# Kernel tuning notes

Hardware: AMD Instinct MI355X
Metric: run time of the kernel (lower is better)

The kernel has to match this reference:

```python
import jax, jax.numpy as jnp
import numpy as np

N_NODES = 50000
N_EDGES = 600000
IN_F = 256
OUT_F = 128


def setup_inputs() -> dict:
    key = jax.random.key(0)
    k1, k2, k3, k4, k5, k6 = jax.random.split(key, 6)
    x = jax.random.normal(k1, (N_NODES, IN_F), dtype=jnp.float32)
    edge_rows = jax.random.randint(k2, (N_EDGES,), 0, N_NODES, dtype=jnp.int32)
    edge_cols = jax.random.randint(k3, (N_EDGES,), 0, N_NODES, dtype=jnp.int32)
    edge_vals = jax.random.uniform(k4, (N_EDGES,), dtype=jnp.float32)
    # xavier_uniform init bound for weight [in, out]
    bound = float(np.sqrt(6.0 / (IN_F + OUT_F)))
    weight = jax.random.uniform(k5, (IN_F, OUT_F), dtype=jnp.float32, minval=-bound, maxval=bound)
    bias = jax.random.normal(k6, (OUT_F,), dtype=jnp.float32) * 0.02
    return {"x": x, "edge_rows": edge_rows, "edge_cols": edge_cols,
            "edge_vals": edge_vals, "weight": weight, "bias": bias}


def reference(x, edge_rows, edge_cols, edge_vals, weight, bias):
    # support = x @ W            [N, out]
    support = x @ weight
    # sparse adj @ support: out[r] += val * support[c] for each edge (r, c, val)
    msgs = edge_vals[:, None] * support[edge_cols]           # [E, out]
    agg = jax.ops.segment_sum(msgs, edge_rows, num_segments=N_NODES)  # [N, out]
    return agg + bias
```

## Files before the change

### kernel.cpp

```cpp
#include <hip/hip_runtime.h>
#include <hip/hip_bf16.h>

#define N_NODES 50000
#define N_EDGES 600000
#define IN_F 256
#define OUT_F 128
#define GEMM_BLOCKS 196
#define NBUCK 782
#define NBUCKA 784
#define BROWS 64
#define NBLK_E 256
#define EPB 2344
#define ITERS 5
#define CAP 1024

typedef __bf16 bf16x8 __attribute__((ext_vector_type(8)));
typedef __bf16 bf16x4 __attribute__((ext_vector_type(4)));
typedef __bf16 bf16x2 __attribute__((ext_vector_type(2)));
typedef float  f32x4  __attribute__((ext_vector_type(4)));

#define GLOAD(P, ks)                                    \
    P##_0 = *(const float4*)(xp0 + (ks) * 32);          \
    P##_1 = *(const float4*)(xp0 + (ks) * 32 + 4);      \
    P##_2 = *(const float4*)(xp1 + (ks) * 32);          \
    P##_3 = *(const float4*)(xp1 + (ks) * 32 + 4);

#define KSTEP(P, ks) {                                                             \
    bf16x8 af0 = { (__bf16)P##_0.x, (__bf16)P##_0.y, (__bf16)P##_0.z, (__bf16)P##_0.w, \
                   (__bf16)P##_1.x, (__bf16)P##_1.y, (__bf16)P##_1.z, (__bf16)P##_1.w };\
    bf16x8 af1 = { (__bf16)P##_2.x, (__bf16)P##_2.y, (__bf16)P##_2.z, (__bf16)P##_2.w, \
                   (__bf16)P##_3.x, (__bf16)P##_3.y, (__bf16)P##_3.z, (__bf16)P##_3.w };\
    _Pragma("unroll")                                                              \
    for (int nt = 0; nt < 8; nt++) {                                               \
        int nrow = nt * 16 + m;                                                    \
        const bf16x8 bf = *(const bf16x8*)(smem + (nrow << 9) +                    \
                            (((ks) * 64 + quad * 16) ^ ((nrow & 7) << 4)));        \
        acc0[nt] = __builtin_amdgcn_mfma_f32_16x16x32_bf16(af0, bf, acc0[nt], 0, 0, 0); \
        acc1[nt] = __builtin_amdgcn_mfma_f32_16x16x32_bf16(af1, bf, acc1[nt], 0, 0, 0); \
    } }

__global__ __launch_bounds__(512, 3) void gcn_gemm_scatter(const float* __restrict__ x,
                                                           const float* __restrict__ w,
                                                           __bf16* __restrict__ support,
                                                           const int* __restrict__ erows,
                                                           const int* __restrict__ ecols,
                                                           const float* __restrict__ evals,
                                                           int* __restrict__ cursor,
                                                           int2* __restrict__ bucketed) {
    __shared__ char smem[65536];
    const int t = threadIdx.x;

    if (blockIdx.x >= GEMM_BLOCKS) {
        int b = blockIdx.x - GEMM_BLOCKS;
        int* lh = (int*)smem;
        for (int j = t; j < NBUCKA; j += 512) lh[j] = 0;
        __syncthreads();
        int e0 = b * EPB;
        int e1 = e0 + EPB; if (e1 > N_EDGES) e1 = N_EDGES;
        int myr[ITERS];
#pragma unroll
        for (int j = 0; j < ITERS; j++) {
            int e = e0 + j * 512 + t;
            myr[j] = -1;
            if (e < e1) {
                int r = erows[e];
                myr[j] = r;
                atomicAdd(&lh[r >> 6], 1);
            }
        }
        __syncthreads();
        for (int j0 = t; j0 < NBUCKA; j0 += 512) {
            int c = lh[j0];
            lh[j0] = c ? atomicAdd(&cursor[j0], c) : 0;
        }
        __syncthreads();
#pragma unroll
        for (int j = 0; j < ITERS; j++) {
            int r = myr[j];
            if (r >= 0) {
                int e = e0 + j * 512 + t;
                int g = r >> 6;
                int rank = atomicAdd(&lh[g], 1);
                if (rank < CAP)
                    bucketed[((size_t)g << 10) + rank] =
                        make_int2(((r & 63) << 16) | ecols[e],
                                  __float_as_int(evals[e]));
            }
        }
        return;
    }

    const int wave = t >> 6;
    const int lane = t & 63;
    const int m    = lane & 15;
    const int quad = lane >> 4;

    {
        int n  = t & 127;
        int kb = (t >> 7) * 4;
        int xorv = (n & 7) << 4;
        char* ldsrow = smem + (n << 9);
#pragma unroll 4
        for (int j = 0; j < 16; j++) {
            int k = kb + 16 * j;
            float a0 = w[(k + 0) * OUT_F + n];
            float a1 = w[(k + 1) * OUT_F + n];
            float a2 = w[(k + 2) * OUT_F + n];
            float a3 = w[(k + 3) * OUT_F + n];
            bf16x4 pk = { (__bf16)a0, (__bf16)a1, (__bf16)a2, (__bf16)a3 };
            *(bf16x4*)(ldsrow + ((2 * k) ^ xorv)) = pk;
        }
    }

    const int row0 = blockIdx.x * 256 + wave * 32;
    int r0 = row0 + m;
    int r1 = row0 + 16 + m;
    const float* xp0 = x + (size_t)(r0 < N_NODES ? r0 : 0) * IN_F + quad * 8;
    const float* xp1 = x + (size_t)(r1 < N_NODES ? r1 : 0) * IN_F + quad * 8;

    f32x4 acc0[8], acc1[8];
#pragma unroll
    for (int nt = 0; nt < 8; nt++) {
        acc0[nt] = (f32x4){0.f, 0.f, 0.f, 0.f};
        acc1[nt] = (f32x4){0.f, 0.f, 0.f, 0.f};
    }

    __syncthreads();

    float4 A_0, A_1, A_2, A_3, B_0, B_1, B_2, B_3, C_0, C_1, C_2, C_3;
    GLOAD(A, 0) GLOAD(B, 1)
    GLOAD(C, 2) KSTEP(A, 0)
    GLOAD(A, 3) KSTEP(B, 1)
    GLOAD(B, 4) KSTEP(C, 2)
    GLOAD(C, 5) KSTEP(A, 3)
    GLOAD(A, 6) KSTEP(B, 4)
    GLOAD(B, 7) KSTEP(C, 5)
    KSTEP(A, 6)
    KSTEP(B, 7)

    __syncthreads();
#pragma unroll
    for (int nt = 0; nt < 8; nt++) {
        int cb = (nt * 16 + m) * 2;
#pragma unroll
        for (int r = 0; r < 4; r++) {
            int lr0 = wave * 32 + quad * 4 + r;
            int lr1 = lr0 + 16;
            *(__bf16*)(smem + (lr0 << 8) + (cb ^ ((lr0 & 7) << 4))) = (__bf16)acc0[nt][r];
            *(__bf16*)(smem + (lr1 << 8) + (cb ^ ((lr1 & 7) << 4))) = (__bf16)acc1[nt][r];
        }
    }
    __syncthreads();
    {
        int row  = t >> 1;
        int half = t & 1;
        int g = blockIdx.x * 256 + row;
        if (g < N_NODES) {
            char* dst = (char*)(support + (size_t)g * OUT_F) + half * 128;
#pragma unroll
            for (int j = 0; j < 8; j++) {
                int boff = (half * 128 + j * 16) ^ ((row & 7) << 4);
                *(bf16x8*)(dst + j * 16) = *(const bf16x8*)(smem + (row << 8) + boff);
            }
        }
    }
}

__global__ __launch_bounds__(512, 8) void gcn_agg_sorted(const __bf16* __restrict__ support,
                                                         const int2* __restrict__ bucketed,
                                                         const int* __restrict__ cursor,
                                                         const float* __restrict__ bias,
                                                         float* __restrict__ out) {
    __shared__ int2 se_raw[CAP];
    __shared__ int2 se[CAP];
    __shared__ int  lh[BROWS];
    __shared__ int  rs[BROWS];
    __shared__ int  run[BROWS];
    __shared__ int  sc[128];
    const int g  = blockIdx.x;
    const int t  = threadIdx.x;
    const int wv = t >> 6, ln = t & 63;

    const int beg = g << 10;
    int ne = cursor[g]; if (ne > CAP) ne = CAP; if (ne < 0) ne = 0;

    if (t < BROWS) lh[t] = 0;
    __syncthreads();
    for (int i = t; i < ne; i += 512) {
        int2 cv = bucketed[beg + i];
        se_raw[i] = cv;
        atomicAdd(&lh[cv.x >> 16], 1);
    }
    __syncthreads();

    if (t < 128) {
        int v = (t < BROWS) ? lh[t] : 0;
        sc[t] = v;
    }
    __syncthreads();
#pragma unroll
    for (int off = 1; off < BROWS; off <<= 1) {
        int x = 0;
        if (t < 128 && t >= off) x = sc[t - off];
        __syncthreads();
        if (t < 128) sc[t] += x;
        __syncthreads();
    }
    if (t < BROWS) {
        int v = lh[t];
        rs[t] = sc[t] - v;
        run[t] = sc[t] - v;
    }
    __syncthreads();

    for (int i = t; i < ne; i += 512) {
        int2 cv = se_raw[i];
        int p = atomicAdd(&run[cv.x >> 16], 1);
        se[p] = make_int2(cv.x & 0xFFFF, cv.y);
    }
    __syncthreads();

    const int grow0 = g * BROWS;
    const __bf16* spL = support + ln * 2;
    const float2 bias2 = *(const float2*)&bias[ln * 2];
    for (int rr = 0; rr < 8; rr++) {
        int row  = wv * 8 + rr;
        int grow = grow0 + row;
        if (grow >= N_NODES) break;
        float2 acc = bias2;
        float2 accB = make_float2(0.f, 0.f);
        int b0 = rs[row];
        int b1 = b0 + lh[row];
        int j = b0;
        for (; j + 7 < b1; j += 8) {
            int2 e0 = se[j];
            int2 e1 = se[j + 1];
            int2 e2 = se[j + 2];
            int2 e3 = se[j + 3];
            int2 e4 = se[j + 4];
            int2 e5 = se[j + 5];
            int2 e6 = se[j + 6];
            int2 e7 = se[j + 7];
            bf16x2 s0 = *(const bf16x2*)(spL + (size_t)e0.x * OUT_F);
            bf16x2 s1 = *(const bf16x2*)(spL + (size_t)e1.x * OUT_F);
            bf16x2 s2 = *(const bf16x2*)(spL + (size_t)e2.x * OUT_F);
            bf16x2 s3 = *(const bf16x2*)(spL + (size_t)e3.x * OUT_F);
            bf16x2 s4 = *(const bf16x2*)(spL + (size_t)e4.x * OUT_F);
            bf16x2 s5 = *(const bf16x2*)(spL + (size_t)e5.x * OUT_F);
            bf16x2 s6 = *(const bf16x2*)(spL + (size_t)e6.x * OUT_F);
            bf16x2 s7 = *(const bf16x2*)(spL + (size_t)e7.x * OUT_F);
            float v0 = __int_as_float(e0.y);
            float v1 = __int_as_float(e1.y);
            float v2 = __int_as_float(e2.y);
            float v3 = __int_as_float(e3.y);
            float v4 = __int_as_float(e4.y);
            float v5 = __int_as_float(e5.y);
            float v6 = __int_as_float(e6.y);
            float v7 = __int_as_float(e7.y);
            acc.x  += v0 * (float)s0.x + v1 * (float)s1.x;
            acc.y  += v0 * (float)s0.y + v1 * (float)s1.y;
            accB.x += v2 * (float)s2.x + v3 * (float)s3.x;
            accB.y += v2 * (float)s2.y + v3 * (float)s3.y;
            acc.x  += v4 * (float)s4.x + v5 * (float)s5.x;
            acc.y  += v4 * (float)s4.y + v5 * (float)s5.y;
            accB.x += v6 * (float)s6.x + v7 * (float)s7.x;
            accB.y += v6 * (float)s6.y + v7 * (float)s7.y;
        }
        for (; j + 3 < b1; j += 4) {
            int2 e0 = se[j];
            int2 e1 = se[j + 1];
            int2 e2 = se[j + 2];
            int2 e3 = se[j + 3];
            bf16x2 s0 = *(const bf16x2*)(spL + (size_t)e0.x * OUT_F);
            bf16x2 s1 = *(const bf16x2*)(spL + (size_t)e1.x * OUT_F);
            bf16x2 s2 = *(const bf16x2*)(spL + (size_t)e2.x * OUT_F);
            bf16x2 s3 = *(const bf16x2*)(spL + (size_t)e3.x * OUT_F);
            float v0 = __int_as_float(e0.y);
            float v1 = __int_as_float(e1.y);
            float v2 = __int_as_float(e2.y);
            float v3 = __int_as_float(e3.y);
            acc.x  += v0 * (float)s0.x + v1 * (float)s1.x;
            acc.y  += v0 * (float)s0.y + v1 * (float)s1.y;
            accB.x += v2 * (float)s2.x + v3 * (float)s3.x;
            accB.y += v2 * (float)s2.y + v3 * (float)s3.y;
        }
        for (; j < b1; j++) {
            int2 e0 = se[j];
            bf16x2 s0 = *(const bf16x2*)(spL + (size_t)e0.x * OUT_F);
            float v0 = __int_as_float(e0.y);
            acc.x += v0 * (float)s0.x;
            acc.y += v0 * (float)s0.y;
        }
        acc.x += accB.x;
        acc.y += accB.y;
        *(float2*)&out[(size_t)grow * OUT_F + ln * 2] = acc;
    }
}

static inline size_t align_up(size_t v, size_t a) { return (v + a - 1) & ~(a - 1); }

extern "C" void kernel_launch(void* const* d_in, const int* in_sizes, int n_in,
                              void* d_out, int out_size, void* d_ws, size_t ws_size,
                              hipStream_t stream) {
    const float* x     = (const float*)d_in[0];
    const int*   erows = (const int*)d_in[1];
    const int*   ecols = (const int*)d_in[2];
    const float* evals = (const float*)d_in[3];
    const float* w     = (const float*)d_in[4];
    const float* bias  = (const float*)d_in[5];
    float* out = (float*)d_out;

    size_t off = 0;
    __bf16* support   = (__bf16*)((char*)d_ws + off);
    off = align_up(off + (size_t)N_NODES * OUT_F * 2, 64);
    int*    cursor    = (int*)((char*)d_ws + off);
    off = align_up(off + (size_t)NBUCKA * 4, 64);
    int2*   bucketed  = (int2*)((char*)d_ws + off);

    hipMemsetAsync(cursor, 0, (size_t)NBUCKA * sizeof(int), stream);

    gcn_gemm_scatter<<<GEMM_BLOCKS + NBLK_E, 512, 0, stream>>>(
        x, w, support, erows, ecols, evals, cursor, bucketed);

    gcn_agg_sorted<<<NBUCK, 512, 0, stream>>>(support, bucketed, cursor, bias, out);
}
```

Before: 142.5 us.

## Halve per-block rows in GEMM and split aggregation buckets across two blocks

The GEMM phase now gives each wave 16 rows instead of 32, so twice as many blocks are launched but each reuses the staged weight tile half as often. The aggregation kernel launches two blocks per 64-row bucket. Each block keeps only the edges for its 32-row half, which adds an overflow cap. The goal is more parallelism on a GPU with many CUs, at the cost of re-staging the weights more often and scanning each bucket's edge list twice.

```diff
diff --git a/kernel.cpp b/kernel.cpp
--- a/kernel.cpp
+++ b/kernel.cpp
@@ -5,14 +5,16 @@
 #define N_EDGES 600000
 #define IN_F 256
 #define OUT_F 128
-#define GEMM_BLOCKS 196
+#define GEMM_BLOCKS 392
 #define NBUCK 782
 #define NBUCKA 784
 #define BROWS 64
+#define AGG_BLOCKS 1564
 #define NBLK_E 256
 #define EPB 2344
 #define ITERS 5
 #define CAP 1024
+#define HCAP 512
 
 typedef __bf16 bf16x8 __attribute__((ext_vector_type(8)));
 typedef __bf16 bf16x4 __attribute__((ext_vector_type(4)));
@@ -21,22 +23,17 @@
 
 #define GLOAD(P, ks)                                    \
     P##_0 = *(const float4*)(xp0 + (ks) * 32);          \
-    P##_1 = *(const float4*)(xp0 + (ks) * 32 + 4);      \
-    P##_2 = *(const float4*)(xp1 + (ks) * 32);          \
-    P##_3 = *(const float4*)(xp1 + (ks) * 32 + 4);
+    P##_1 = *(const float4*)(xp0 + (ks) * 32 + 4);
 
 #define KSTEP(P, ks) {                                                             \
     bf16x8 af0 = { (__bf16)P##_0.x, (__bf16)P##_0.y, (__bf16)P##_0.z, (__bf16)P##_0.w, \
                    (__bf16)P##_1.x, (__bf16)P##_1.y, (__bf16)P##_1.z, (__bf16)P##_1.w };\
-    bf16x8 af1 = { (__bf16)P##_2.x, (__bf16)P##_2.y, (__bf16)P##_2.z, (__bf16)P##_2.w, \
-                   (__bf16)P##_3.x, (__bf16)P##_3.y, (__bf16)P##_3.z, (__bf16)P##_3.w };\
     _Pragma("unroll")                                                              \
     for (int nt = 0; nt < 8; nt++) {                                               \
         int nrow = nt * 16 + m;                                                    \
         const bf16x8 bf = *(const bf16x8*)(smem + (nrow << 9) +                    \
                             (((ks) * 64 + quad * 16) ^ ((nrow & 7) << 4)));        \
         acc0[nt] = __builtin_amdgcn_mfma_f32_16x16x32_bf16(af0, bf, acc0[nt], 0, 0, 0); \
-        acc1[nt] = __builtin_amdgcn_mfma_f32_16x16x32_bf16(af1, bf, acc1[nt], 0, 0, 0); \
     } }
 
 __global__ __launch_bounds__(512, 3) void gcn_gemm_scatter(const float* __restrict__ x,
@@ -112,22 +109,18 @@
         }
     }
 
-    const int row0 = blockIdx.x * 256 + wave * 32;
+    const int row0 = blockIdx.x * 128 + wave * 16;
     int r0 = row0 + m;
-    int r1 = row0 + 16 + m;
     const float* xp0 = x + (size_t)(r0 < N_NODES ? r0 : 0) * IN_F + quad * 8;
-    const float* xp1 = x + (size_t)(r1 < N_NODES ? r1 : 0) * IN_F + quad * 8;
-
-    f32x4 acc0[8], acc1[8];
-#pragma unroll
-    for (int nt = 0; nt < 8; nt++) {
+
+    f32x4 acc0[8];
+#pragma unroll
+    for (int nt = 0; nt < 8; nt++)
         acc0[nt] = (f32x4){0.f, 0.f, 0.f, 0.f};
-        acc1[nt] = (f32x4){0.f, 0.f, 0.f, 0.f};
-    }
-
-    __syncthreads();
-
-    float4 A_0, A_1, A_2, A_3, B_0, B_1, B_2, B_3, C_0, C_1, C_2, C_3;
+
+    __syncthreads();
+
+    float4 A_0, A_1, B_0, B_1, C_0, C_1;
     GLOAD(A, 0) GLOAD(B, 1)
     GLOAD(C, 2) KSTEP(A, 0)
     GLOAD(A, 3) KSTEP(B, 1)
@@ -144,22 +137,20 @@
         int cb = (nt * 16 + m) * 2;
 #pragma unroll
         for (int r = 0; r < 4; r++) {
-            int lr0 = wave * 32 + quad * 4 + r;
-            int lr1 = lr0 + 16;
+            int lr0 = wave * 16 + quad * 4 + r;
             *(__bf16*)(smem + (lr0 << 8) + (cb ^ ((lr0 & 7) << 4))) = (__bf16)acc0[nt][r];
-            *(__bf16*)(smem + (lr1 << 8) + (cb ^ ((lr1 & 7) << 4))) = (__bf16)acc1[nt][r];
         }
     }
     __syncthreads();
     {
-        int row  = t >> 1;
-        int half = t & 1;
-        int g = blockIdx.x * 256 + row;
+        int row = t >> 2;
+        int q   = t & 3;
+        int g = blockIdx.x * 128 + row;
         if (g < N_NODES) {
-            char* dst = (char*)(support + (size_t)g * OUT_F) + half * 128;
-#pragma unroll
-            for (int j = 0; j < 8; j++) {
-                int boff = (half * 128 + j * 16) ^ ((row & 7) << 4);
+            char* dst = (char*)(support + (size_t)g * OUT_F) + q * 64;
+#pragma unroll
+            for (int j = 0; j < 4; j++) {
+                int boff = (q * 64 + j * 16) ^ ((row & 7) << 4);
                 *(bf16x8*)(dst + j * 16) = *(const bf16x8*)(smem + (row << 8) + boff);
             }
         }
@@ -171,66 +162,75 @@
                                                          const int* __restrict__ cursor,
                                                          const float* __restrict__ bias,
                                                          float* __restrict__ out) {
-    __shared__ int2 se_raw[CAP];
-    __shared__ int2 se[CAP];
-    __shared__ int  lh[BROWS];
-    __shared__ int  rs[BROWS];
-    __shared__ int  run[BROWS];
-    __shared__ int  sc[128];
-    const int g  = blockIdx.x;
+    __shared__ int2 se_raw[HCAP];
+    __shared__ int2 se[HCAP];
+    __shared__ int  lh[32];
+    __shared__ int  rs[32];
+    __shared__ int  run[32];
+    __shared__ int  sc[64];
+    __shared__ int  cnt;
+    const int g  = blockIdx.x >> 1;
+    const int h  = blockIdx.x & 1;
     const int t  = threadIdx.x;
     const int wv = t >> 6, ln = t & 63;
 
     const int beg = g << 10;
     int ne = cursor[g]; if (ne > CAP) ne = CAP; if (ne < 0) ne = 0;
 
-    if (t < BROWS) lh[t] = 0;
+    if (t == 0) cnt = 0;
+    if (t < 32) lh[t] = 0;
     __syncthreads();
     for (int i = t; i < ne; i += 512) {
         int2 cv = bucketed[beg + i];
-        se_raw[i] = cv;
-        atomicAdd(&lh[cv.x >> 16], 1);
-    }
-    __syncthreads();
-
-    if (t < 128) {
-        int v = (t < BROWS) ? lh[t] : 0;
-        sc[t] = v;
-    }
-    __syncthreads();
-#pragma unroll
-    for (int off = 1; off < BROWS; off <<= 1) {
+        int lr = cv.x >> 16;
+        if ((lr >> 5) == h) {
+            int p = atomicAdd(&cnt, 1);
+            if (p < HCAP) {
+                se_raw[p] = cv;
+                atomicAdd(&lh[lr & 31], 1);
+            }
+        }
+    }
+    __syncthreads();
+
+    int nm = cnt; if (nm > HCAP) nm = HCAP;
+
+    if (t < 64) sc[t] = (t < 32) ? lh[t] : 0;
+    __syncthreads();
+#pragma unroll
+    for (int off = 1; off < 32; off <<= 1) {
         int x = 0;
-        if (t < 128 && t >= off) x = sc[t - off];
-        __syncthreads();
-        if (t < 128) sc[t] += x;
-        __syncthreads();
-    }
-    if (t < BROWS) {
+        if (t < 64 && t >= off) x = sc[t - off];
+        __syncthreads();
+        if (t < 64) sc[t] += x;
+        __syncthreads();
+    }
+    if (t < 32) {
         int v = lh[t];
         rs[t] = sc[t] - v;
         run[t] = sc[t] - v;
     }
     __syncthreads();
 
-    for (int i = t; i < ne; i += 512) {
-        int2 cv = se_raw[i];
-        int p = atomicAdd(&run[cv.x >> 16], 1);
-        se[p] = make_int2(cv.x & 0xFFFF, cv.y);
-    }
-    __syncthreads();
-
-    const int grow0 = g * BROWS;
+    if (t < nm) {
+        int2 cv = se_raw[t];
+        int p = atomicAdd(&run[(cv.x >> 16) & 31], 1);
+        if (p < HCAP)
+            se[p] = make_int2(cv.x & 0xFFFF, cv.y);
+    }
+    __syncthreads();
+
+    const int grow0 = g * BROWS + h * 32;
     const __bf16* spL = support + ln * 2;
     const float2 bias2 = *(const float2*)&bias[ln * 2];
-    for (int rr = 0; rr < 8; rr++) {
-        int row  = wv * 8 + rr;
+    for (int rr = 0; rr < 4; rr++) {
+        int row  = wv * 4 + rr;
         int grow = grow0 + row;
         if (grow >= N_NODES) break;
         float2 acc = bias2;
         float2 accB = make_float2(0.f, 0.f);
         int b0 = rs[row];
-        int b1 = b0 + lh[row];
+        int b1 = b0 + lh[row]; if (b1 > nm) b1 = nm;
         int j = b0;
         for (; j + 7 < b1; j += 8) {
             int2 e0 = se[j];
@@ -322,5 +322,5 @@
     gcn_gemm_scatter<<<GEMM_BLOCKS + NBLK_E, 512, 0, stream>>>(
         x, w, support, erows, ecols, evals, cursor, bucketed);
 
-    gcn_agg_sorted<<<NBUCK, 512, 0, stream>>>(support, bucketed, cursor, bias, out);
+    gcn_agg_sorted<<<AGG_BLOCKS, 512, 0, stream>>>(support, bucketed, cursor, bias, out);
 }
```

New measurement: 145.1 us. About the same (+1.9%).
